# Optimization experiments

Measured on AMD Instinct MI355X. Metric: run time of the kernel, lower is better.

The kernel has to match this reference:

```python
import jax, jax.numpy as jnp
import numpy as np
import math

B, T, F_ = 4, 1024, 1024
TO_DIM, FROM_DIM, LATENT, H = 1024, 1024, 1024, 16
HEAD_DIM = LATENT // H

def _linear_params(key, in_dim, out_dim):
    kw, kb = jax.random.split(key)
    bound = 1.0 / math.sqrt(in_dim)
    W = jax.random.uniform(kw, (out_dim, in_dim), minval=-bound, maxval=bound, dtype=jnp.float32)
    b = jax.random.uniform(kb, (out_dim,), minval=-bound, maxval=bound, dtype=jnp.float32)
    return W, b

def setup_inputs() -> dict:
    key = jax.random.key(0)
    ks = jax.random.split(key, 7)
    X_to = jax.random.normal(ks[0], (B, T, TO_DIM), dtype=jnp.float32)
    X_from = jax.random.normal(ks[1], (B, F_, FROM_DIM), dtype=jnp.float32)
    mask_from = jax.random.randint(ks[2], (B, T, F_), 0, 2, dtype=jnp.int32)
    Wq, bq = _linear_params(ks[3], TO_DIM, LATENT)
    Wk, bk = _linear_params(ks[4], FROM_DIM, LATENT)
    Wv, bv = _linear_params(ks[5], FROM_DIM, LATENT)
    Wo, bo = _linear_params(ks[6], LATENT, TO_DIM)
    return {"X_to": X_to, "X_from": X_from, "mask_from": mask_from,
            "Wq": Wq, "bq": bq, "Wk": Wk, "bk": bk, "Wv": Wv, "bv": bv, "Wo": Wo, "bo": bo}

def _split_heads(x):
    # [b, t, (h k)] -> [b, h, t, k]
    b, t, _ = x.shape
    return x.reshape(b, t, H, HEAD_DIM).transpose(0, 2, 1, 3)

def reference(X_to, X_from, mask_from, Wq, bq, Wk, bk, Wv, bv, Wo, bo):
    Q = _split_heads(X_to @ Wq.T + bq)
    # NOTE: source swaps names — K comes from v_linear, V from k_linear. Reproduced literally.
    K = _split_heads(X_from @ Wv.T + bv)
    V = _split_heads(X_from @ Wk.T + bk)
    attn = jnp.einsum('bhtk,bhfk->bhtf', Q, K) / math.sqrt(HEAD_DIM)
    attn = jnp.where(mask_from[:, None, :, :] == 0, jnp.float32(-10000.0), attn)
    attn = jax.nn.softmax(attn, axis=-1)
    out = jnp.einsum('bhtf,bhfk->bhtk', attn, V)  # [b,h,t,k]
    out = out.transpose(0, 2, 1, 3).reshape(X_to.shape[0], X_to.shape[1], LATENT)
    return out @ Wo.T + bo
```

## Files before the change

kernel.cpp:

```cpp
#include <hip/hip_runtime.h>
#include <hip/hip_bf16.h>
#include <math.h>

#define BB 4
#define TT 1024
#define FF 1024
#define DIM 1024
#define NH 16
#define HD 64
#define MROWS (BB * TT)
#define FB (FF / 64)

typedef __attribute__((ext_vector_type(8))) short short8;
typedef __attribute__((ext_vector_type(4))) short short4v;
typedef __attribute__((ext_vector_type(4))) float f32x4;
typedef __hip_bfloat16 bf16;

__device__ __forceinline__ void async_copy16(const void* g, void* l) {
    __builtin_amdgcn_global_load_lds((const __attribute__((address_space(1))) void*)g,
                                     (__attribute__((address_space(3))) void*)l,
                                     16, 0, 0);
}

struct ConvArgs {
    const float* src[6];
    bf16* dst[6];
    int nvec[6];
    int blk_end[6];
    const int* mask;
    unsigned long long* Mb;
};

__global__ __launch_bounds__(256) void convert_pack(ConvArgs a) {
    int bx = blockIdx.x;
    if (bx >= a.blk_end[5]) {
        const int lane = threadIdx.x & 63;
        const int waveId = (bx - a.blk_end[5]) * 4 + (threadIdx.x >> 6);
#pragma unroll
        for (int it = 0; it < 16; ++it) {
            int c = waveId * 16 + it;
            int v = a.mask[(size_t)c * 64 + lane];
            unsigned long long bits = __ballot(v != 0);
            if (lane == 0) a.Mb[c] = bits;
        }
        return;
    }
    int seg = 0;
#pragma unroll
    for (int k = 0; k < 5; ++k) if (bx >= a.blk_end[k]) seg = k + 1;
    int b0 = seg ? a.blk_end[seg - 1] : 0;
    int idx = (bx - b0) * 256 + threadIdx.x;
    if (idx >= a.nvec[seg]) return;
    float4 v = ((const float4*)a.src[seg])[idx];
    union { bf16 t[4]; ushort4 u; } o;
    o.t[0] = __float2bfloat16(v.x);
    o.t[1] = __float2bfloat16(v.y);
    o.t[2] = __float2bfloat16(v.z);
    o.t[3] = __float2bfloat16(v.w);
    *(ushort4*)(a.dst[seg] + 4 * (size_t)idx) = o.u;
}

#define BK 64

struct QkvArgs {
    const bf16* A[3]; const bf16* W[3]; const float* bias[3]; bf16* C[3];
    int N[3]; int biasRow[3];
};

#define BARRIER() __builtin_amdgcn_s_barrier()

__global__ __launch_bounds__(512) void gemm_qkv(QkvArgs q) {
    __shared__ bf16 lds[67584];

    const int op = blockIdx.y;
    const bf16* A = q.A[op];
    const bf16* W = q.W[op];
    const float* bias = q.bias[op];
    bf16* C = q.C[op];
    const int N = q.N[op];
    const int brow = q.biasRow[op];

    const int lin = blockIdx.x;
    const int xcd = lin & 7;
    const int t8  = lin >> 3;
    int mt, nt;
    if (brow) { mt = t8 & 3; nt = xcd * 2 + (t8 >> 2); }
    else      { mt = xcd * 2 + (t8 >> 2); nt = t8 & 3; }
    const int m0 = mt * 256, n0 = nt * 256;

    const int tid  = threadIdx.x;
    const int lane = tid & 63;
    const int wave = tid >> 6;
    const int quad = lane >> 4;
    const int l16  = lane & 15;
    const int wm   = wave >> 2;
    const int wn   = wave & 3;
    const int wbase = tid & ~63;

    const int srow = tid >> 3;
    const int scol = (tid & 7) ^ (srow & 7);
    const bf16* pA = A + (size_t)(m0 + srow) * DIM + scol * 8;
    const bf16* pB = W + (size_t)(n0 + srow) * DIM + scol * 8;

#define STAGE(P, ISB, TTL, HH) do { \
    const bf16* s_ = (P) + (size_t)(HH) * (128 * DIM) + (TTL) * 64; \
    bf16* d_ = lds + ((TTL) & 1) * 32768 + (ISB) * 16384 + (HH) * 8192 + wbase * 8; \
    async_copy16(s_, d_); \
    async_copy16(s_ + 64 * DIM, d_ + 4096); \
} while (0)

    f32x4 acc[8][4] = {};
    short8 a[4][2], b[4][2];

    STAGE(pA, 0, 0, 0); STAGE(pB, 1, 0, 0);
    STAGE(pA, 0, 0, 1); STAGE(pB, 1, 0, 1);
    STAGE(pA, 0, 1, 0); STAGE(pB, 1, 1, 0);
    asm volatile("s_waitcnt vmcnt(4)");
    BARRIER();

#define LDA(AH) do { \
    _Pragma("unroll") for (int miq = 0; miq < 4; ++miq) { \
        int r_ = (AH) * 128 + wm * 64 + miq * 16 + l16; \
        const bf16* ba_ = Ab + r_ * 64; \
        a[miq][0] = *(const short8*)(ba_ + ((quad ^ (r_ & 7)) * 8)); \
        a[miq][1] = *(const short8*)(ba_ + (((quad + 4) ^ (r_ & 7)) * 8)); \
    } } while (0)

#define LDB(BH) do { \
    _Pragma("unroll") for (int niq = 0; niq < 2; ++niq) { \
        int r_ = (BH) * 128 + wn * 32 + niq * 16 + l16; \
        const bf16* bb_ = Bb + r_ * 64; \
        b[(BH) * 2 + niq][0] = *(const short8*)(bb_ + ((quad ^ (r_ & 7)) * 8)); \
        b[(BH) * 2 + niq][1] = *(const short8*)(bb_ + (((quad + 4) ^ (r_ & 7)) * 8)); \
    } } while (0)

#define MMA(AH, BH) do { \
    _Pragma("unroll") for (int miq = 0; miq < 4; ++miq) \
    _Pragma("unroll") for (int niq = 0; niq < 2; ++niq) { \
        f32x4& c_ = acc[(AH) * 4 + miq][(BH) * 2 + niq]; \
        c_ = __builtin_amdgcn_mfma_f32_16x16x32_bf16(a[miq][0], b[(BH) * 2 + niq][0], c_, 0, 0, 0); \
        c_ = __builtin_amdgcn_mfma_f32_16x16x32_bf16(a[miq][1], b[(BH) * 2 + niq][1], c_, 0, 0, 0); \
    } } while (0)

#define PHASE_MFMA(AH, BH) do { \
    BARRIER(); \
    __builtin_amdgcn_s_setprio(1); \
    MMA(AH, BH); \
    __builtin_amdgcn_s_setprio(0); \
} while (0)

#pragma unroll 2
    for (int t = 0; t < 16; ++t) {
        const bf16* Ab = lds + (t & 1) * 32768;
        const bf16* Bb = Ab + 16384;

        LDA(0); LDB(0);
        if (t + 1 < 16) STAGE(pA, 0, t + 1, 1);
        PHASE_MFMA(0, 0);
        BARRIER();

        LDB(1);
        if (t + 1 < 16) STAGE(pB, 1, t + 1, 1);
        PHASE_MFMA(0, 1);
        BARRIER();

        LDA(1);
        if (t + 2 < 16) STAGE(pA, 0, t + 2, 0);
        PHASE_MFMA(1, 0);
        BARRIER();

        if (t + 2 < 16) STAGE(pB, 1, t + 2, 0);
        PHASE_MFMA(1, 1);
        if (t < 14)       { asm volatile("s_waitcnt vmcnt(4)"); }
        else if (t == 14) { asm volatile("s_waitcnt vmcnt(0)"); }
        BARRIER();
    }

    bf16* Cs = lds;
#pragma unroll
    for (int ni = 0; ni < 4; ++ni) {
        const int nl = (ni >> 1) * 128 + wn * 32 + (ni & 1) * 16 + l16;
        float bcol = brow ? 0.0f : bias[n0 + nl];
#pragma unroll
        for (int mi = 0; mi < 8; ++mi)
#pragma unroll
            for (int i = 0; i < 4; ++i) {
                const int ml = (mi >> 2) * 128 + wm * 64 + (mi & 3) * 16 + quad * 4 + i;
                float v = acc[mi][ni][i] + (brow ? bias[m0 + ml] : bcol);
                Cs[ml * 264 + nl] = __float2bfloat16(v);
            }
    }
    __syncthreads();
#pragma unroll
    for (int j = 0; j < 16; ++j) {
        int slot = j * 512 + tid;
        int rr = slot >> 5, cc = slot & 31;
        short8 v = *(const short8*)(Cs + rr * 264 + cc * 8);
        *(short8*)(C + (size_t)(m0 + rr) * N + n0 + cc * 8) = v;
    }
#undef STAGE
#undef LDA
#undef LDB
#undef MMA
#undef PHASE_MFMA
}

__global__ __launch_bounds__(256) void gemm_o(
    const bf16* __restrict__ A, const bf16* __restrict__ W,
    const float* __restrict__ bias, float* __restrict__ C)
{
    __shared__ float smemf[128 * 66];
    bf16* As = (bf16*)smemf;
    bf16* Bs = As + 128 * BK;

    const int lin = blockIdx.x + 16 * blockIdx.y;
    const int xcd = lin & 7;
    const int t   = lin >> 3;
    const int m0 = (xcd * 4 + (t >> 4)) * 128;
    const int n0 = (((t & 15) + 2 * xcd) & 15) * 64;

    const int tid  = threadIdx.x;
    const int lane = tid & 63;
    const int wave = tid >> 6;
    const int quad = lane >> 4;
    const int l16  = lane & 15;
    const int wm = wave & 1;
    const int wn = wave >> 1;
    const int wbase = tid & ~63;

    f32x4 acc[4][2] = {};

    for (int k0 = 0; k0 < DIM; k0 += BK) {
#pragma unroll
        for (int j = 0; j < 4; ++j) {
            int slot = j * 256 + tid;
            int r = slot >> 3;
            int g = (slot & 7) ^ (r & 7);
            async_copy16(A + (size_t)(m0 + r) * DIM + k0 + g * 8,
                         As + (size_t)(j * 256 + wbase) * 8);
        }
#pragma unroll
        for (int j = 0; j < 2; ++j) {
            int slot = j * 256 + tid;
            int r = slot >> 3;
            int g = (slot & 7) ^ (r & 7);
            async_copy16(W + (size_t)(n0 + r) * DIM + k0 + g * 8,
                         Bs + (size_t)(j * 256 + wbase) * 8);
        }
        __syncthreads();

#pragma unroll
        for (int kk = 0; kk < 2; ++kk) {
            short8 a[4], b[2];
#pragma unroll
            for (int mi = 0; mi < 4; ++mi) {
                int r = wm * 64 + mi * 16 + l16;
                int p = (kk * 4 + quad) ^ (r & 7);
                a[mi] = *(const short8*)(As + r * BK + p * 8);
            }
#pragma unroll
            for (int ni = 0; ni < 2; ++ni) {
                int r = wn * 32 + ni * 16 + l16;
                int p = (kk * 4 + quad) ^ (r & 7);
                b[ni] = *(const short8*)(Bs + r * BK + p * 8);
            }
#pragma unroll
            for (int mi = 0; mi < 4; ++mi)
#pragma unroll
                for (int ni = 0; ni < 2; ++ni)
                    acc[mi][ni] = __builtin_amdgcn_mfma_f32_16x16x32_bf16(
                        a[mi], b[ni], acc[mi][ni], 0, 0, 0);
        }
        __syncthreads();
    }

    float* Cs = smemf;
#pragma unroll
    for (int ni = 0; ni < 2; ++ni) {
        const int nl = wn * 32 + ni * 16 + l16;
        const float bcol = bias[n0 + nl];
#pragma unroll
        for (int mi = 0; mi < 4; ++mi)
#pragma unroll
            for (int i = 0; i < 4; ++i) {
                const int ml = wm * 64 + mi * 16 + quad * 4 + i;
                Cs[ml * 66 + nl] = acc[mi][ni][i] + bcol;
            }
    }
    __syncthreads();
#pragma unroll
    for (int j = 0; j < 8; ++j) {
        int slot = j * 256 + tid;
        int rr = slot >> 4, cc = slot & 15;
        float4 v = *(const float4*)(Cs + rr * 66 + cc * 4);
        *(float4*)(C + (size_t)(m0 + rr) * DIM + n0 + cc * 4) = v;
    }
}

__global__ __launch_bounds__(256, 4) void attn_kernel(
    const bf16* Qg, const bf16* __restrict__ Kg, const bf16* __restrict__ Vtg,
    const unsigned long long* __restrict__ Mbits, bf16* Og)
{
    __shared__ bf16 Ks[128 * 64];
    __shared__ bf16 Vts[64 * 128];
    __shared__ bf16 Pt[64 * 136];
    __shared__ float ls[64];

    const int tid  = threadIdx.x;
    const int lane = tid & 63;
    const int wave = tid >> 6;
    const int quad = lane >> 4;
    const int l16  = lane & 15;

    const int lin = blockIdx.x + 16 * (blockIdx.y + 16 * blockIdx.z);
    const int xcd = lin & 7;
    const int t   = lin >> 3;
    const int bh  = xcd * 8 + (t >> 4);
    const int b   = bh >> 4;
    const int h   = bh & 15;
    const int t0  = (t & 15) * 64;

    const size_t qrow0 = (size_t)b * TT + t0;
    const size_t krow0 = (size_t)b * FF;
    const int wbase = tid & ~63;
    const int myrow = wave * 16 + l16;

    const bf16* qptr = Qg + (qrow0 + myrow) * DIM + h * HD;
    short8 qb0 = *(const short8*)(qptr + quad * 8);
    short8 qb1 = *(const short8*)(qptr + 32 + quad * 8);

    const unsigned long long* mrow = Mbits + (qrow0 + myrow) * FB;
    unsigned long long w0 = mrow[0];
    unsigned long long w1 = mrow[1];

    float lsum = 0.f;
    f32x4 oacc[4] = {};

#pragma unroll 1
    for (int it = 0; it < 8; ++it) {
        const int f0 = it * 128;
#pragma unroll
        for (int j = 0; j < 4; ++j) {
            int slot = j * 256 + tid;
            int rk = slot >> 3;
            int gk = (slot & 7) ^ (rk & 7);
            async_copy16(Kg + (krow0 + f0 + rk) * DIM + h * HD + gk * 8,
                         Ks + (size_t)(j * 256 + wbase) * 8);
            int rv = slot >> 4;
            int gv = (slot & 15) ^ (rv & 15);
            async_copy16(Vtg + (size_t)(h * HD + rv) * MROWS + b * FF + f0 + gv * 8,
                         Vts + (size_t)(j * 256 + wbase) * 8);
        }
        unsigned long long nw0 = 0, nw1 = 0;
        if (it < 7) { nw0 = mrow[2 * it + 2]; nw1 = mrow[2 * it + 3]; }
        __syncthreads();

        f32x4 sacc[8];
#pragma unroll
        for (int ft = 0; ft < 8; ++ft) {
            int r = ft * 16 + l16;
            short8 ka0 = *(const short8*)(Ks + r * 64 + ((quad       ^ (r & 7)) * 8));
            short8 ka1 = *(const short8*)(Ks + r * 64 + (((quad + 4) ^ (r & 7)) * 8));
            f32x4 s = {};
            s = __builtin_amdgcn_mfma_f32_16x16x32_bf16(ka0, qb0, s, 0, 0, 0);
            s = __builtin_amdgcn_mfma_f32_16x16x32_bf16(ka1, qb1, s, 0, 0, 0);
            sacc[ft] = s;
        }

#pragma unroll
        for (int ft = 0; ft < 8; ++ft) {
            const unsigned long long word = (ft < 4) ? w0 : w1;
            const unsigned bits4 =
                (unsigned)(word >> ((ft & 3) * 16 + quad * 4)) & 0xFu;
            union { short4v v; short s[4]; } pk;
            float psum = 0.f;
#pragma unroll
            for (int i = 0; i < 4; ++i) {
                float p = (bits4 >> i) & 1u ? __expf(sacc[ft][i] * 0.125f) : 0.f;
                psum += p;
                pk.s[i] = (short)__bfloat16_as_ushort(__float2bfloat16(p));
            }
            lsum += psum;
            *(short4v*)(Pt + myrow * 136 + ft * 16 + quad * 4) = pk.v;
        }
        w0 = nw0; w1 = nw1;

        short8 pa[4];
#pragma unroll
        for (int kf = 0; kf < 4; ++kf)
            pa[kf] = *(const short8*)(Pt + myrow * 136 + kf * 32 + quad * 8);
#pragma unroll
        for (int nt = 0; nt < 4; ++nt) {
            int rd = nt * 16 + l16;
#pragma unroll
            for (int kf = 0; kf < 4; ++kf) {
                int g = (kf * 4 + quad) ^ (rd & 15);
                short8 vb = *(const short8*)(Vts + rd * 128 + g * 8);
                oacc[nt] = __builtin_amdgcn_mfma_f32_16x16x32_bf16(pa[kf], vb, oacc[nt], 0, 0, 0);
            }
        }
        __syncthreads();
    }

    lsum += __shfl_xor(lsum, 16);
    lsum += __shfl_xor(lsum, 32);
    if (quad == 0) ls[myrow] = lsum;

#pragma unroll
    for (int i = 0; i < 4; ++i) {
        float inv = 1.0f / ls[wave * 16 + quad * 4 + i];
        const int prow = wave * 16 + quad * 4 + i;
#pragma unroll
        for (int nt = 0; nt < 4; ++nt)
            Pt[prow * 136 + nt * 16 + l16] = __float2bfloat16(oacc[nt][i] * inv);
    }
    __syncthreads();
#pragma unroll
    for (int j = 0; j < 2; ++j) {
        int s = j * 256 + tid;
        int rr = s >> 3, off = (s & 7) * 8;
        short8 v = *(const short8*)(Pt + rr * 136 + off);
        *(short8*)(Og + (qrow0 + rr) * DIM + h * HD + off) = v;
    }
}

extern "C" void kernel_launch(void* const* d_in, const int* in_sizes, int n_in,
                              void* d_out, int out_size, void* d_ws, size_t ws_size,
                              hipStream_t stream) {
    const float* X_to   = (const float*)d_in[0];
    const float* X_from = (const float*)d_in[1];
    const int*   mask   = (const int*)  d_in[2];
    const float* Wq     = (const float*)d_in[3];
    const float* bq     = (const float*)d_in[4];
    const float* Wk     = (const float*)d_in[5];
    const float* bk     = (const float*)d_in[6];
    const float* Wv     = (const float*)d_in[7];
    const float* bv     = (const float*)d_in[8];
    const float* Wo     = (const float*)d_in[9];
    const float* bo     = (const float*)d_in[10];
    float* out = (float*)d_out;

    char* ws = (char*)d_ws;
    bf16* Xt16 = (bf16*)(ws);
    bf16* Xf16 = (bf16*)(ws + (8u  << 20));
    bf16* Wq16 = (bf16*)(ws + (16u << 20));
    bf16* Wv16 = (bf16*)(ws + (18u << 20));
    bf16* Wk16 = (bf16*)(ws + (20u << 20));
    bf16* Wo16 = (bf16*)(ws + (22u << 20));
    bf16* Q16  = (bf16*)(ws + (24u << 20));
    bf16* K16  = (bf16*)(ws + (32u << 20));
    bf16* Vt16 = (bf16*)(ws + (40u << 20));
    unsigned long long* Mb = (unsigned long long*)(ws + (48u << 20));

    ConvArgs ca;
    ca.src[0] = X_to;   ca.dst[0] = Xt16; ca.nvec[0] = MROWS * DIM / 4;
    ca.src[1] = X_from; ca.dst[1] = Xf16; ca.nvec[1] = MROWS * DIM / 4;
    ca.src[2] = Wq;     ca.dst[2] = Wq16; ca.nvec[2] = DIM * DIM / 4;
    ca.src[3] = Wv;     ca.dst[3] = Wv16; ca.nvec[3] = DIM * DIM / 4;
    ca.src[4] = Wk;     ca.dst[4] = Wk16; ca.nvec[4] = DIM * DIM / 4;
    ca.src[5] = Wo;     ca.dst[5] = Wo16; ca.nvec[5] = DIM * DIM / 4;
    int cum = 0;
    for (int k = 0; k < 6; ++k) { cum += ca.nvec[k] / 256; ca.blk_end[k] = cum; }
    ca.mask = mask; ca.Mb = Mb;
    convert_pack<<<cum + 1024, 256, 0, stream>>>(ca);

    QkvArgs qa;
    qa.A[0] = Xt16; qa.W[0] = Wq16; qa.bias[0] = bq; qa.C[0] = Q16;
    qa.N[0] = DIM; qa.biasRow[0] = 0;
    qa.A[1] = Xf16; qa.W[1] = Wv16; qa.bias[1] = bv; qa.C[1] = K16;
    qa.N[1] = DIM; qa.biasRow[1] = 0;
    qa.A[2] = Wk16; qa.W[2] = Xf16; qa.bias[2] = bk; qa.C[2] = Vt16;
    qa.N[2] = MROWS; qa.biasRow[2] = 1;
    gemm_qkv<<<dim3(64, 3), 512, 0, stream>>>(qa);

    attn_kernel<<<dim3(TT / 64, NH, BB), 256, 0, stream>>>(
        Q16, K16, Vt16, Mb, Q16);

    gemm_o<<<dim3(DIM / 64, MROWS / 128), 256, 0, stream>>>(Q16, Wo16, bo, out);
}
```

Measured before the change: 223.5 us.

## Double-buffer K/V tiles in attention and fold softmax scale into Q projection

```diff
diff --git a/kernel.cpp b/kernel.cpp
--- a/kernel.cpp
+++ b/kernel.cpp
@@ -64,7 +64,7 @@
 
 struct QkvArgs {
     const bf16* A[3]; const bf16* W[3]; const float* bias[3]; bf16* C[3];
-    int N[3]; int biasRow[3];
+    int N[3]; int biasRow[3]; float scale[3];
 };
 
 #define BARRIER() __builtin_amdgcn_s_barrier()
@@ -79,6 +79,7 @@
     bf16* C = q.C[op];
     const int N = q.N[op];
     const int brow = q.biasRow[op];
+    const float sc = q.scale[op];
 
     const int lin = blockIdx.x;
     const int xcd = lin & 7;
@@ -186,7 +187,7 @@
 #pragma unroll
             for (int i = 0; i < 4; ++i) {
                 const int ml = (mi >> 2) * 128 + wm * 64 + (mi & 3) * 16 + quad * 4 + i;
-                float v = acc[mi][ni][i] + (brow ? bias[m0 + ml] : bcol);
+                float v = (acc[mi][ni][i] + (brow ? bias[m0 + ml] : bcol)) * sc;
                 Cs[ml * 264 + nl] = __float2bfloat16(v);
             }
     }
@@ -297,13 +298,13 @@
     }
 }
 
-__global__ __launch_bounds__(256, 4) void attn_kernel(
+__global__ __launch_bounds__(256, 3) void attn_kernel(
     const bf16* Qg, const bf16* __restrict__ Kg, const bf16* __restrict__ Vtg,
     const unsigned long long* __restrict__ Mbits, bf16* Og)
 {
-    __shared__ bf16 Ks[128 * 64];
-    __shared__ bf16 Vts[64 * 128];
-    __shared__ bf16 Pt[64 * 136];
+    __shared__ bf16 Ks[2 * 64 * 64];
+    __shared__ bf16 Vts[2 * 64 * 64];
+    __shared__ bf16 Pt[64 * 72];
     __shared__ float ls[64];
 
     const int tid  = threadIdx.x;
@@ -329,78 +330,94 @@
     short8 qb0 = *(const short8*)(qptr + quad * 8);
     short8 qb1 = *(const short8*)(qptr + 32 + quad * 8);
 
+    const int srow = tid >> 3;
+    const int sg   = ((tid & 7) ^ (srow & 7)) * 8;
+    const bf16* kS = Kg + (krow0 + srow) * DIM + h * HD + sg;
+    const bf16* vS = Vtg + (size_t)(h * HD + srow) * MROWS + b * FF + sg;
+
+#define STAGE_KV(BUF, IT) do { \
+    const bf16* ks_ = kS + (size_t)((IT) * 64) * DIM; \
+    const bf16* vs_ = vS + (IT) * 64; \
+    bf16* kd_ = Ks + (BUF) * 4096 + wbase * 8; \
+    bf16* vd_ = Vts + (BUF) * 4096 + wbase * 8; \
+    async_copy16(ks_, kd_); \
+    async_copy16(ks_ + (size_t)32 * DIM, kd_ + 2048); \
+    async_copy16(vs_, vd_); \
+    async_copy16(vs_ + (size_t)32 * MROWS, vd_ + 2048); \
+} while (0)
+
     const unsigned long long* mrow = Mbits + (qrow0 + myrow) * FB;
-    unsigned long long w0 = mrow[0];
-    unsigned long long w1 = mrow[1];
+    unsigned long long w = mrow[0];
 
     float lsum = 0.f;
     f32x4 oacc[4] = {};
 
-#pragma unroll 1
-    for (int it = 0; it < 8; ++it) {
-        const int f0 = it * 128;
-#pragma unroll
-        for (int j = 0; j < 4; ++j) {
-            int slot = j * 256 + tid;
-            int rk = slot >> 3;
-            int gk = (slot & 7) ^ (rk & 7);
-            async_copy16(Kg + (krow0 + f0 + rk) * DIM + h * HD + gk * 8,
-                         Ks + (size_t)(j * 256 + wbase) * 8);
-            int rv = slot >> 4;
-            int gv = (slot & 15) ^ (rv & 15);
-            async_copy16(Vtg + (size_t)(h * HD + rv) * MROWS + b * FF + f0 + gv * 8,
-                         Vts + (size_t)(j * 256 + wbase) * 8);
-        }
-        unsigned long long nw0 = 0, nw1 = 0;
-        if (it < 7) { nw0 = mrow[2 * it + 2]; nw1 = mrow[2 * it + 3]; }
-        __syncthreads();
-
-        f32x4 sacc[8];
-#pragma unroll
-        for (int ft = 0; ft < 8; ++ft) {
+    STAGE_KV(0, 0);
+    STAGE_KV(1, 1);
+    asm volatile("s_waitcnt vmcnt(4)");
+    BARRIER();
+
+#pragma unroll 2
+    for (int it = 0; it < 16; ++it) {
+        const bf16* Kc = Ks + (it & 1) * 4096;
+        const bf16* Vc = Vts + (it & 1) * 4096;
+
+        unsigned long long nw = (it < 15) ? mrow[it + 1] : 0;
+
+        f32x4 sacc[4];
+        __builtin_amdgcn_s_setprio(1);
+#pragma unroll
+        for (int ft = 0; ft < 4; ++ft) {
             int r = ft * 16 + l16;
-            short8 ka0 = *(const short8*)(Ks + r * 64 + ((quad       ^ (r & 7)) * 8));
-            short8 ka1 = *(const short8*)(Ks + r * 64 + (((quad + 4) ^ (r & 7)) * 8));
+            short8 ka0 = *(const short8*)(Kc + r * 64 + ((quad       ^ (r & 7)) * 8));
+            short8 ka1 = *(const short8*)(Kc + r * 64 + (((quad + 4) ^ (r & 7)) * 8));
             f32x4 s = {};
             s = __builtin_amdgcn_mfma_f32_16x16x32_bf16(ka0, qb0, s, 0, 0, 0);
             s = __builtin_amdgcn_mfma_f32_16x16x32_bf16(ka1, qb1, s, 0, 0, 0);
             sacc[ft] = s;
         }
-
-#pragma unroll
-        for (int ft = 0; ft < 8; ++ft) {
-            const unsigned long long word = (ft < 4) ? w0 : w1;
+        __builtin_amdgcn_s_setprio(0);
+
+#pragma unroll
+        for (int ft = 0; ft < 4; ++ft) {
             const unsigned bits4 =
-                (unsigned)(word >> ((ft & 3) * 16 + quad * 4)) & 0xFu;
+                (unsigned)(w >> (ft * 16 + quad * 4)) & 0xFu;
             union { short4v v; short s[4]; } pk;
             float psum = 0.f;
 #pragma unroll
             for (int i = 0; i < 4; ++i) {
-                float p = (bits4 >> i) & 1u ? __expf(sacc[ft][i] * 0.125f) : 0.f;
+                float p = (bits4 >> i) & 1u ? __expf(sacc[ft][i]) : 0.f;
                 psum += p;
                 pk.s[i] = (short)__bfloat16_as_ushort(__float2bfloat16(p));
             }
             lsum += psum;
-            *(short4v*)(Pt + myrow * 136 + ft * 16 + quad * 4) = pk.v;
-        }
-        w0 = nw0; w1 = nw1;
-
-        short8 pa[4];
-#pragma unroll
-        for (int kf = 0; kf < 4; ++kf)
-            pa[kf] = *(const short8*)(Pt + myrow * 136 + kf * 32 + quad * 8);
+            *(short4v*)(Pt + myrow * 72 + ft * 16 + quad * 4) = pk.v;
+        }
+        w = nw;
+
+        short8 pa[2];
+        pa[0] = *(const short8*)(Pt + myrow * 72 + quad * 8);
+        pa[1] = *(const short8*)(Pt + myrow * 72 + 32 + quad * 8);
+        __builtin_amdgcn_s_setprio(1);
 #pragma unroll
         for (int nt = 0; nt < 4; ++nt) {
             int rd = nt * 16 + l16;
 #pragma unroll
-            for (int kf = 0; kf < 4; ++kf) {
-                int g = (kf * 4 + quad) ^ (rd & 15);
-                short8 vb = *(const short8*)(Vts + rd * 128 + g * 8);
+            for (int kf = 0; kf < 2; ++kf) {
+                int g = (kf * 4 + quad) ^ (rd & 7);
+                short8 vb = *(const short8*)(Vc + rd * 64 + g * 8);
                 oacc[nt] = __builtin_amdgcn_mfma_f32_16x16x32_bf16(pa[kf], vb, oacc[nt], 0, 0, 0);
             }
         }
-        __syncthreads();
-    }
+        __builtin_amdgcn_s_setprio(0);
+
+        BARRIER();
+        if (it + 2 < 16) STAGE_KV(it & 1, it + 2);
+        if (it < 14)       { asm volatile("s_waitcnt vmcnt(4)"); }
+        else if (it == 14) { asm volatile("s_waitcnt vmcnt(0)"); }
+        BARRIER();
+    }
+#undef STAGE_KV
 
     lsum += __shfl_xor(lsum, 16);
     lsum += __shfl_xor(lsum, 32);
@@ -412,14 +429,14 @@
         const int prow = wave * 16 + quad * 4 + i;
 #pragma unroll
         for (int nt = 0; nt < 4; ++nt)
-            Pt[prow * 136 + nt * 16 + l16] = __float2bfloat16(oacc[nt][i] * inv);
+            Pt[prow * 72 + nt * 16 + l16] = __float2bfloat16(oacc[nt][i] * inv);
     }
     __syncthreads();
 #pragma unroll
     for (int j = 0; j < 2; ++j) {
         int s = j * 256 + tid;
         int rr = s >> 3, off = (s & 7) * 8;
-        short8 v = *(const short8*)(Pt + rr * 136 + off);
+        short8 v = *(const short8*)(Pt + rr * 72 + off);
         *(short8*)(Og + (qrow0 + rr) * DIM + h * HD + off) = v;
     }
 }
@@ -466,11 +483,11 @@
 
     QkvArgs qa;
     qa.A[0] = Xt16; qa.W[0] = Wq16; qa.bias[0] = bq; qa.C[0] = Q16;
-    qa.N[0] = DIM; qa.biasRow[0] = 0;
+    qa.N[0] = DIM; qa.biasRow[0] = 0; qa.scale[0] = 0.125f;
     qa.A[1] = Xf16; qa.W[1] = Wv16; qa.bias[1] = bv; qa.C[1] = K16;
-    qa.N[1] = DIM; qa.biasRow[1] = 0;
+    qa.N[1] = DIM; qa.biasRow[1] = 0; qa.scale[1] = 1.0f;
     qa.A[2] = Wk16; qa.W[2] = Xf16; qa.bias[2] = bk; qa.C[2] = Vt16;
-    qa.N[2] = MROWS; qa.biasRow[2] = 1;
+    qa.N[2] = MROWS; qa.biasRow[2] = 1; qa.scale[2] = 1.0f;
     gemm_qkv<<<dim3(64, 3), 512, 0, stream>>>(qa);
 
     attn_kernel<<<dim3(TT / 64, NH, BB), 256, 0, stream>>>(
```

Measured after the change: 225.2 us. About the same (+0.8%).
